# Kernel tuning notes

Hardware: AMD Instinct MI355X
Metric: run time of the kernel (lower is better)

Reference implementation:

```python
import jax, jax.numpy as jnp
import numpy as np

N = 100000
NEG_SLOPE = 0.2
EPS = 1e-16


def _leaky_relu(x):
    return jnp.where(x > 0, x, NEG_SLOPE * x)


def gat_conv(x, src, dst, W, a_src, a_dst, b, heads, out_ch):
    # x: [N, F_in], W: [F_in, heads*out_ch], a_src/a_dst: [heads, out_ch], b: [heads*out_ch]
    h = (x @ W).reshape(N, heads, out_ch)                     # [N, H, C]
    alpha_s = jnp.einsum('nhc,hc->nh', h, a_src)              # [N, H]
    alpha_d = jnp.einsum('nhc,hc->nh', h, a_dst)              # [N, H]
    e = _leaky_relu(alpha_s[src] + alpha_d[dst])              # [E, H]
    # softmax over incoming edges per destination node
    m = jax.ops.segment_max(e, dst, num_segments=N)           # [N, H]
    ee = jnp.exp(e - m[dst])
    denom = jax.ops.segment_sum(ee, dst, num_segments=N)      # [N, H]
    alpha = ee / (denom[dst] + EPS)                           # [E, H]
    msg = h[src] * alpha[:, :, None]                          # [E, H, C]
    out = jax.ops.segment_sum(msg, dst, num_segments=N)       # [N, H, C]
    return out.reshape(N, heads * out_ch) + b


def setup_inputs() -> dict:
    key = jax.random.key(0)
    ks = jax.random.split(key, 16)
    x = jax.random.normal(ks[0], (N, 128), dtype=jnp.float32)
    edge_index = jax.random.randint(ks[1], (2, 1600000), 0, N, dtype=jnp.int64)
    s = 0.1
    return {
        'x': x,
        'edge_index': edge_index,
        'W0': jax.random.normal(ks[2], (128, 4 * 32), dtype=jnp.float32) * s,
        'asrc0': jax.random.normal(ks[3], (4, 32), dtype=jnp.float32) * s,
        'adst0': jax.random.normal(ks[4], (4, 32), dtype=jnp.float32) * s,
        'b0': jnp.zeros((128,), dtype=jnp.float32),
        'W1': jax.random.normal(ks[5], (128, 4 * 32), dtype=jnp.float32) * s,
        'asrc1': jax.random.normal(ks[6], (4, 32), dtype=jnp.float32) * s,
        'adst1': jax.random.normal(ks[7], (4, 32), dtype=jnp.float32) * s,
        'b1': jnp.zeros((128,), dtype=jnp.float32),
        'W2': jax.random.normal(ks[8], (128, 1 * 32), dtype=jnp.float32) * s,
        'asrc2': jax.random.normal(ks[9], (1, 32), dtype=jnp.float32) * s,
        'adst2': jax.random.normal(ks[10], (1, 32), dtype=jnp.float32) * s,
        'b2': jnp.zeros((32,), dtype=jnp.float32),
    }


def reference(x, edge_index, W0, asrc0, adst0, b0, W1, asrc1, adst1, b1, W2, asrc2, adst2, b2):
    # PyG GATConv default add_self_loops=True
    loops = jnp.arange(N, dtype=edge_index.dtype)
    src = jnp.concatenate([edge_index[0], loops])
    dst = jnp.concatenate([edge_index[1], loops])
    # dropout layers are identity in eval mode
    h = gat_conv(x, src, dst, W0, asrc0, adst0, b0, heads=4, out_ch=32)
    h = jax.nn.relu(h)
    h = gat_conv(h, src, dst, W1, asrc1, adst1, b1, heads=4, out_ch=32)
    h = jax.nn.relu(h)
    out = gat_conv(h, src, dst, W2, asrc2, adst2, b2, heads=1, out_ch=32)
    return out
```

## Files before the change

### kernel.cpp

```cpp
#include <hip/hip_runtime.h>
#include <hip/hip_fp16.h>

#define NEG_SLOPE 0.2f
#define EPSV 1e-16f
#define NXCD 8
#define BCAP2 448
#define EPB 8192

typedef _Float16 half8 __attribute__((ext_vector_type(8)));
typedef _Float16 half4v __attribute__((ext_vector_type(4)));
typedef float floatx4 __attribute__((ext_vector_type(4)));

__device__ __forceinline__ float leaky_relu(float v) {
    return v > 0.f ? v : NEG_SLOPE * v;
}

__global__ __launch_bounds__(256)
void wconv3_kernel(const float* __restrict__ W0, const float* __restrict__ W1,
                   const float* __restrict__ W2, __half* __restrict__ Wt0,
                   __half* __restrict__ Wt1, __half* __restrict__ Wt2)
{
    const int idx = blockIdx.x * 256 + threadIdx.x;
    if (idx < 16384) {
        const int k = idx >> 7, c = idx & 127;
        Wt0[c * 128 + k] = __float2half(W0[idx]);
    } else if (idx < 32768) {
        const int i = idx - 16384;
        const int k = i >> 7, c = i & 127;
        Wt1[c * 128 + k] = __float2half(W1[i]);
    } else if (idx < 36864) {
        const int i = idx - 32768;
        const int k = i >> 5, c = i & 31;
        Wt2[c * 128 + k] = __float2half(W2[i]);
    }
}

template<int HC, typename XT>
__global__ __launch_bounds__(256)
void mfma_gemm_kernel(const XT* __restrict__ X, const __half* __restrict__ Wt,
                      const float* __restrict__ asrc, const float* __restrict__ adst,
                      __half* __restrict__ Hout, float* __restrict__ as_,
                      float* __restrict__ ad_, int nrows)
{
    constexpr int NH = HC / 32;
    const int wid = (blockIdx.x * 256 + threadIdx.x) >> 6;
    const int lane = threadIdx.x & 63;
    const int row0 = wid * 16;
    if (row0 >= nrows) return;
    const int r = lane & 15;
    const int kq = lane >> 4;
    const int arow = min(row0 + r, nrows - 1);

    half8 a[4];
    #pragma unroll
    for (int kk = 0; kk < 4; ++kk) {
        const int k0 = kk * 32 + kq * 8;
        if constexpr (sizeof(XT) == 4) {
            const float4 f0 = *(const float4*)&X[(size_t)arow * 128 + k0];
            const float4 f1 = *(const float4*)&X[(size_t)arow * 128 + k0 + 4];
            half8 v;
            v[0] = (_Float16)f0.x; v[1] = (_Float16)f0.y;
            v[2] = (_Float16)f0.z; v[3] = (_Float16)f0.w;
            v[4] = (_Float16)f1.x; v[5] = (_Float16)f1.y;
            v[6] = (_Float16)f1.z; v[7] = (_Float16)f1.w;
            a[kk] = v;
        } else {
            a[kk] = *(const half8*)&X[(size_t)arow * 128 + k0];
        }
    }

    float asp[NH][4];
    float adp[NH][4];
    #pragma unroll
    for (int hh = 0; hh < NH; ++hh)
        #pragma unroll
        for (int j = 0; j < 4; ++j) { asp[hh][j] = 0.f; adp[hh][j] = 0.f; }

    #pragma unroll
    for (int ct = 0; ct < HC / 16; ++ct) {
        floatx4 acc = {0.f, 0.f, 0.f, 0.f};
        #pragma unroll
        for (int kk = 0; kk < 4; ++kk) {
            const half8 b = *(const half8*)&Wt[(size_t)(ct * 16 + r) * 128 + kk * 32 + kq * 8];
            acc = __builtin_amdgcn_mfma_f32_16x16x32_f16(a[kk], b, acc, 0, 0, 0);
        }
        const float avs = asrc[ct * 16 + r];
        const float avd = adst[ct * 16 + r];
        #pragma unroll
        for (int j = 0; j < 4; ++j) {
            asp[ct / 2][j] = fmaf(acc[j], avs, asp[ct / 2][j]);
            adp[ct / 2][j] = fmaf(acc[j], avd, adp[ct / 2][j]);
        }
        #pragma unroll
        for (int j = 0; j < 4; ++j) {
            const int orow = row0 + kq * 4 + j;
            if (orow < nrows)
                Hout[(size_t)orow * HC + ct * 16 + r] = __float2half(acc[j]);
        }
    }

    #pragma unroll
    for (int off = 1; off < 16; off <<= 1) {
        #pragma unroll
        for (int hh = 0; hh < NH; ++hh)
            #pragma unroll
            for (int j = 0; j < 4; ++j) {
                asp[hh][j] += __shfl_xor(asp[hh][j], off);
                adp[hh][j] += __shfl_xor(adp[hh][j], off);
            }
    }
    if constexpr (NH == 4) {
        #pragma unroll
        for (int j = 0; j < 4; ++j) {
            const int row = row0 + kq * 4 + j;
            if (row < nrows) {
                #pragma unroll
                for (int hh = 0; hh < 4; ++hh) {
                    if (r == j * 4 + hh) {
                        as_[row * 4 + hh] = asp[hh][j];
                        ad_[row * 4 + hh] = adp[hh][j];
                    }
                }
            }
        }
    } else {
        #pragma unroll
        for (int j = 0; j < 4; ++j) {
            const int row = row0 + kq * 4 + j;
            if (row < nrows) {
                if (r == j)     as_[row] = asp[0][j];
                if (r == j + 8) ad_[row] = adp[0][j];
            }
        }
    }
}

__global__ __launch_bounds__(256)
void bucket_append_kernel(const int* __restrict__ srcs, const int* __restrict__ dsts,
                          int E, int NB, int* __restrict__ bcur,
                          unsigned* __restrict__ packed)
{
    __shared__ int hist[1024];
    __shared__ int cursor[1024];
    const int t = threadIdx.x;
    const int xcd = blockIdx.x & (NXCD - 1);
    const int base = blockIdx.x * EPB;

    for (int i = t; i < NB; i += 256) hist[i] = 0;
    __syncthreads();
    for (int k = 0; k < EPB / 256; ++k) {
        const int e = base + k * 256 + t;
        if (e < E) atomicAdd(&hist[dsts[e] >> 7], 1);
    }
    __syncthreads();
    for (int i = t; i < NB; i += 256) {
        const int c = hist[i];
        cursor[i] = (c > 0) ? atomicAdd(&bcur[i * NXCD + xcd], c) : 0;
    }
    __syncthreads();
    for (int k = 0; k < EPB / 256; ++k) {
        const int e = base + k * 256 + t;
        if (e < E) {
            const int s = srcs[e];
            const int d = dsts[e];
            const int b = d >> 7;
            const int p = atomicAdd(&cursor[b], 1);
            if (p < BCAP2)
                packed[(size_t)(b * NXCD + xcd) * BCAP2 + p] =
                    (unsigned)s | ((unsigned)(d & 127) << 20);
        }
    }
}

__global__ __launch_bounds__(256)
void bucket_count_kernel(const unsigned* __restrict__ packed, const int* __restrict__ bcur,
                         int* __restrict__ counts, int N)
{
    __shared__ int cnt[128];
    const int t = threadIdx.x;
    const int b = blockIdx.x;
    const int nbase = b * 128;
    if (t < 128) cnt[t] = 1;
    __syncthreads();
    for (int x = 0; x < NXCD; ++x) {
        const int sb = b * NXCD + x;
        const int n = min(bcur[sb], BCAP2);
        const unsigned* bp = packed + (size_t)sb * BCAP2;
        for (int i = t; i < n; i += 256)
            atomicAdd(&cnt[bp[i] >> 20], 1);
    }
    __syncthreads();
    if (t < 128 && nbase + t < N) counts[nbase + t] = cnt[t];
}

__global__ __launch_bounds__(256)
void scan1_kernel(const int* __restrict__ in, int* __restrict__ out,
                  int* __restrict__ bsums, int n)
{
    __shared__ int lds[256];
    const int t = threadIdx.x;
    const int base = blockIdx.x * 1024 + t * 4;
    int v0 = 0, v1 = 0, v2 = 0, v3 = 0;
    if (base + 0 < n) v0 = in[base + 0];
    if (base + 1 < n) v1 = in[base + 1];
    if (base + 2 < n) v2 = in[base + 2];
    if (base + 3 < n) v3 = in[base + 3];
    const int tsum = v0 + v1 + v2 + v3;
    lds[t] = tsum;
    __syncthreads();
    for (int off = 1; off < 256; off <<= 1) {
        const int y = (t >= off) ? lds[t - off] : 0;
        __syncthreads();
        lds[t] += y;
        __syncthreads();
    }
    int excl = lds[t] - tsum;
    if (t == 255) bsums[blockIdx.x] = lds[255];
    if (base + 0 < n) out[base + 0] = excl; excl += v0;
    if (base + 1 < n) out[base + 1] = excl; excl += v1;
    if (base + 2 < n) out[base + 2] = excl; excl += v2;
    if (base + 3 < n) out[base + 3] = excl;
}

__global__ __launch_bounds__(256)
void scan2_kernel(int* __restrict__ bsums, int nb)
{
    __shared__ int lds[256];
    const int t = threadIdx.x;
    const int v = (t < nb) ? bsums[t] : 0;
    lds[t] = v;
    __syncthreads();
    for (int off = 1; off < 256; off <<= 1) {
        const int y = (t >= off) ? lds[t - off] : 0;
        __syncthreads();
        lds[t] += y;
        __syncthreads();
    }
    if (t < nb) bsums[t] = lds[t] - v;
}

__global__ __launch_bounds__(256)
void scan3_kernel(int* __restrict__ row_ptr, const int* __restrict__ bsums,
                  int n, int etot)
{
    const int idx = blockIdx.x * 256 + threadIdx.x;
    if (idx < n) row_ptr[idx] += bsums[idx >> 10];
    if (idx == n) row_ptr[n] = etot;
}

__global__ __launch_bounds__(256)
void bucket_scatter_kernel(const unsigned* __restrict__ packed, const int* __restrict__ bcur,
                           const int* __restrict__ row_ptr, int* __restrict__ col, int N)
{
    __shared__ int cur[128];
    const int t = threadIdx.x;
    const int b = blockIdx.x;
    const int nbase = b * 128;
    if (t < 128 && nbase + t < N) cur[t] = row_ptr[nbase + t];
    __syncthreads();
    if (t < 128 && nbase + t < N) {
        const int p = atomicAdd(&cur[t], 1);
        col[p] = nbase + t;
    }
    for (int x = 0; x < NXCD; ++x) {
        const int sb = b * NXCD + x;
        const int n = min(bcur[sb], BCAP2);
        const unsigned* bp = packed + (size_t)sb * BCAP2;
        for (int i = t; i < n; i += 256) {
            const unsigned en = bp[i];
            const int p = atomicAdd(&cur[en >> 20], 1);
            col[p] = en & 0xFFFFF;
        }
    }
}

template<int H>
__global__ __launch_bounds__(256)
void gather_kernel(const int* __restrict__ row_ptr, const int* __restrict__ col,
                   const float* __restrict__ as_, const float* __restrict__ ad_,
                   const __half* __restrict__ hbuf, const float* __restrict__ bias,
                   __half* __restrict__ hin, float* __restrict__ outf, int N)
{
    __shared__ float pS[4][64 * H];
    __shared__ int   sS[4][64];
    const int w = threadIdx.x >> 6;
    const int lane = threadIdx.x & 63;
    const int d = blockIdx.x * 4 + w;
    if (d >= N) return;
    const int jb = __builtin_amdgcn_readfirstlane(row_ptr[d]);
    const int je = __builtin_amdgcn_readfirstlane(row_ptr[d + 1]);

    float ad0 = 0.f, ad1 = 0.f, ad2 = 0.f, ad3 = 0.f;
    if (H == 4) {
        const float4 adv = *(const float4*)&ad_[d * 4];
        ad0 = adv.x; ad1 = adv.y; ad2 = adv.z; ad3 = adv.w;
    } else {
        ad0 = ad_[d];
    }

    float s0 = 0.f, s1 = 0.f, s2 = 0.f, s3 = 0.f;
    float a0 = 0.f, a1 = 0.f, a2 = 0.f, a3 = 0.f;
    float a4 = 0.f, a5 = 0.f, a6 = 0.f, a7 = 0.f;
    const int q4 = lane >> 4;
    const int cq = lane & 15;
    const int h4 = cq >> 2;
    const int q8 = lane >> 3;
    const int c8 = (lane & 7) * 4;

    for (int cb = jb; cb < je; cb += 64) {
        const int j = cb + lane;
        const int cnt = min(64, je - cb);
        int sreg = 0;
        float p0 = 0.f, p1 = 0.f, p2 = 0.f, p3 = 0.f;
        if (j < je) {
            sreg = col[j];
            if (H == 4) {
                const float4 a = *(const float4*)&as_[sreg * 4];
                p0 = __expf(leaky_relu(a.x + ad0)); s0 += p0;
                p1 = __expf(leaky_relu(a.y + ad1)); s1 += p1;
                p2 = __expf(leaky_relu(a.z + ad2)); s2 += p2;
                p3 = __expf(leaky_relu(a.w + ad3)); s3 += p3;
            } else {
                p0 = __expf(leaky_relu(as_[sreg] + ad0)); s0 += p0;
            }
        }
        __builtin_amdgcn_wave_barrier();
        sS[w][lane] = sreg;
        if (H == 4) {
            *(float4*)&pS[w][lane * 4] = make_float4(p0, p1, p2, p3);
        } else {
            pS[w][lane] = p0;
        }
        __builtin_amdgcn_wave_barrier();
        if (H == 4) {
            #pragma unroll 4
            for (int e2 = q4; e2 < cnt; e2 += 4) {
                const int s2v = sS[w][e2];
                const float pp = pS[w][e2 * 4 + h4];
                const half8 v = *(const half8*)&hbuf[(size_t)s2v * 128 + cq * 8];
                a0 = fmaf(pp, (float)v[0], a0);
                a1 = fmaf(pp, (float)v[1], a1);
                a2 = fmaf(pp, (float)v[2], a2);
                a3 = fmaf(pp, (float)v[3], a3);
                a4 = fmaf(pp, (float)v[4], a4);
                a5 = fmaf(pp, (float)v[5], a5);
                a6 = fmaf(pp, (float)v[6], a6);
                a7 = fmaf(pp, (float)v[7], a7);
            }
        } else {
            #pragma unroll 4
            for (int e2 = q8; e2 < cnt; e2 += 8) {
                const int s2v = sS[w][e2];
                const float pp = pS[w][e2];
                const half4v v = *(const half4v*)&hbuf[(size_t)s2v * 32 + c8];
                a0 = fmaf(pp, (float)v[0], a0);
                a1 = fmaf(pp, (float)v[1], a1);
                a2 = fmaf(pp, (float)v[2], a2);
                a3 = fmaf(pp, (float)v[3], a3);
            }
        }
        __builtin_amdgcn_wave_barrier();
    }

    #pragma unroll
    for (int off = 32; off >= 1; off >>= 1) {
        s0 += __shfl_xor(s0, off);
        if (H == 4) {
            s1 += __shfl_xor(s1, off);
            s2 += __shfl_xor(s2, off);
            s3 += __shfl_xor(s3, off);
        }
    }
    if (H == 4) {
        a0 += __shfl_xor(a0, 16); a0 += __shfl_xor(a0, 32);
        a1 += __shfl_xor(a1, 16); a1 += __shfl_xor(a1, 32);
        a2 += __shfl_xor(a2, 16); a2 += __shfl_xor(a2, 32);
        a3 += __shfl_xor(a3, 16); a3 += __shfl_xor(a3, 32);
        a4 += __shfl_xor(a4, 16); a4 += __shfl_xor(a4, 32);
        a5 += __shfl_xor(a5, 16); a5 += __shfl_xor(a5, 32);
        a6 += __shfl_xor(a6, 16); a6 += __shfl_xor(a6, 32);
        a7 += __shfl_xor(a7, 16); a7 += __shfl_xor(a7, 32);
        if (lane < 16) {
            const float sh = (h4 == 0) ? s0 : (h4 == 1) ? s1 : (h4 == 2) ? s2 : s3;
            const float inv = 1.f / (sh + EPSV);
            const int c0 = cq * 8;
            const float4 b0v = *(const float4*)&bias[c0];
            const float4 b1v = *(const float4*)&bias[c0 + 4];
            union { __half2 h2[4]; float4 f4; } u;
            u.h2[0] = __floats2half2_rn(fmaxf(fmaf(a0, inv, b0v.x), 0.f),
                                        fmaxf(fmaf(a1, inv, b0v.y), 0.f));
            u.h2[1] = __floats2half2_rn(fmaxf(fmaf(a2, inv, b0v.z), 0.f),
                                        fmaxf(fmaf(a3, inv, b0v.w), 0.f));
            u.h2[2] = __floats2half2_rn(fmaxf(fmaf(a4, inv, b1v.x), 0.f),
                                        fmaxf(fmaf(a5, inv, b1v.y), 0.f));
            u.h2[3] = __floats2half2_rn(fmaxf(fmaf(a6, inv, b1v.z), 0.f),
                                        fmaxf(fmaf(a7, inv, b1v.w), 0.f));
            *(float4*)&hin[(size_t)d * 128 + c0] = u.f4;
        }
    } else {
        a0 += __shfl_xor(a0, 8); a0 += __shfl_xor(a0, 16); a0 += __shfl_xor(a0, 32);
        a1 += __shfl_xor(a1, 8); a1 += __shfl_xor(a1, 16); a1 += __shfl_xor(a1, 32);
        a2 += __shfl_xor(a2, 8); a2 += __shfl_xor(a2, 16); a2 += __shfl_xor(a2, 32);
        a3 += __shfl_xor(a3, 8); a3 += __shfl_xor(a3, 16); a3 += __shfl_xor(a3, 32);
        if (lane < 8) {
            const float inv = 1.f / (s0 + EPSV);
            const float4 bb = *(const float4*)&bias[c8];
            *(float4*)&outf[(size_t)d * 32 + c8] =
                make_float4(fmaf(a0, inv, bb.x), fmaf(a1, inv, bb.y),
                            fmaf(a2, inv, bb.z), fmaf(a3, inv, bb.w));
        }
    }
}

extern "C" void kernel_launch(void* const* d_in, const int* in_sizes, int n_in,
                              void* d_out, int out_size, void* d_ws, size_t ws_size,
                              hipStream_t stream)
{
    const float* x     = (const float*)d_in[0];
    const int*   ei    = (const int*)d_in[1];
    const float* W0    = (const float*)d_in[2];
    const float* asrc0 = (const float*)d_in[3];
    const float* adst0 = (const float*)d_in[4];
    const float* b0    = (const float*)d_in[5];
    const float* W1    = (const float*)d_in[6];
    const float* asrc1 = (const float*)d_in[7];
    const float* adst1 = (const float*)d_in[8];
    const float* b1    = (const float*)d_in[9];
    const float* W2    = (const float*)d_in[10];
    const float* asrc2 = (const float*)d_in[11];
    const float* adst2 = (const float*)d_in[12];
    const float* b2    = (const float*)d_in[13];

    const int N = in_sizes[0] / 128;
    const int E = in_sizes[1] / 2;
    const int Etot = E + N;
    const int NB = (N + 127) / 128;
    const int* srcs = ei;
    const int* dsts = ei + E;

    __half* hbuf    = (__half*)d_ws;
    __half* hin     = hbuf + (size_t)N * 128;
    float* as_      = (float*)(hin + (size_t)N * 128);
    float* ad_      = as_ + (size_t)N * 4;
    __half* Wt0     = (__half*)(ad_ + (size_t)N * 4);
    __half* Wt1     = Wt0 + 128 * 128;
    __half* Wt2     = Wt1 + 128 * 128;
    int* counts     = (int*)(Wt2 + 32 * 128);
    int* row_ptr    = counts + N;
    int* bsums      = row_ptr + N + 1;
    int* col        = bsums + 256;
    int* bcur       = col + Etot;
    unsigned* packed = (unsigned*)(bcur + NB * NXCD);

    const dim3 blk(256);
    const int gemm_grid    = ((N + 15) / 16 + 3) / 4;
    const int append_grid  = (E + EPB - 1) / EPB;
    const int gather_grid  = (N + 3) / 4;
    const int nb1          = (N + 1023) / 1024;

    wconv3_kernel<<<(36864 + 255) / 256, blk, 0, stream>>>(W0, W1, W2, Wt0, Wt1, Wt2);
    hipMemsetAsync(bcur, 0, (size_t)NB * NXCD * 4, stream);
    bucket_append_kernel<<<append_grid, blk, 0, stream>>>(srcs, dsts, E, NB, bcur, packed);
    bucket_count_kernel<<<NB, blk, 0, stream>>>(packed, bcur, counts, N);
    scan1_kernel<<<nb1, blk, 0, stream>>>(counts, row_ptr, bsums, N);
    scan2_kernel<<<1, blk, 0, stream>>>(bsums, nb1);
    scan3_kernel<<<(N + 1 + 255) / 256, blk, 0, stream>>>(row_ptr, bsums, N, Etot);
    bucket_scatter_kernel<<<NB, blk, 0, stream>>>(packed, bcur, row_ptr, col, N);

    mfma_gemm_kernel<128, float><<<gemm_grid, blk, 0, stream>>>(
        x, Wt0, asrc0, adst0, hbuf, as_, ad_, N);
    gather_kernel<4><<<gather_grid, blk, 0, stream>>>(row_ptr, col, as_, ad_, hbuf, b0, hin, nullptr, N);

    mfma_gemm_kernel<128, __half><<<gemm_grid, blk, 0, stream>>>(
        hin, Wt1, asrc1, adst1, hbuf, as_, ad_, N);
    gather_kernel<4><<<gather_grid, blk, 0, stream>>>(row_ptr, col, as_, ad_, hbuf, b1, hin, nullptr, N);

    mfma_gemm_kernel<32, __half><<<gemm_grid, blk, 0, stream>>>(
        hin, Wt2, asrc2, adst2, hbuf, as_, ad_, N);
    gather_kernel<1><<<gather_grid, blk, 0, stream>>>(row_ptr, col, as_, ad_, hbuf, b2, nullptr, (float*)d_out, N);
}
```

Baseline: 370.3 us.

## Fold CSR build into fewer kernels and widen final-layer gather loads

```diff
diff --git a/kernel.cpp b/kernel.cpp
--- a/kernel.cpp
+++ b/kernel.cpp
@@ -8,7 +8,6 @@
 #define EPB 8192
 
 typedef _Float16 half8 __attribute__((ext_vector_type(8)));
-typedef _Float16 half4v __attribute__((ext_vector_type(4)));
 typedef float floatx4 __attribute__((ext_vector_type(4)));
 
 __device__ __forceinline__ float leaky_relu(float v) {
@@ -18,9 +17,11 @@
 __global__ __launch_bounds__(256)
 void wconv3_kernel(const float* __restrict__ W0, const float* __restrict__ W1,
                    const float* __restrict__ W2, __half* __restrict__ Wt0,
-                   __half* __restrict__ Wt1, __half* __restrict__ Wt2)
+                   __half* __restrict__ Wt1, __half* __restrict__ Wt2,
+                   int* __restrict__ bcur, int nbx)
 {
     const int idx = blockIdx.x * 256 + threadIdx.x;
+    if (idx < nbx) bcur[idx] = 0;
     if (idx < 16384) {
         const int k = idx >> 7, c = idx & 127;
         Wt0[c * 128 + k] = __float2half(W0[idx]);
@@ -173,15 +174,55 @@
 }
 
 __global__ __launch_bounds__(256)
-void bucket_count_kernel(const unsigned* __restrict__ packed, const int* __restrict__ bcur,
-                         int* __restrict__ counts, int N)
+void scanB_kernel(const int* __restrict__ bcur, int* __restrict__ bbase,
+                  int* __restrict__ row_ptr, int NB, int N)
+{
+    __shared__ int lds[256];
+    const int t = threadIdx.x;
+    int v0 = 0, v1 = 0, v2 = 0, v3 = 0;
+    #pragma unroll
+    for (int j = 0; j < 4; ++j) {
+        const int i = t * 4 + j;
+        int s = 0;
+        if (i < NB) {
+            s = min(128, N - i * 128);
+            #pragma unroll
+            for (int x = 0; x < NXCD; ++x)
+                s += min(bcur[i * NXCD + x], BCAP2);
+        }
+        if (j == 0) v0 = s; else if (j == 1) v1 = s; else if (j == 2) v2 = s; else v3 = s;
+    }
+    const int tsum = v0 + v1 + v2 + v3;
+    lds[t] = tsum;
+    __syncthreads();
+    for (int off = 1; off < 256; off <<= 1) {
+        const int y = (t >= off) ? lds[t - off] : 0;
+        __syncthreads();
+        lds[t] += y;
+        __syncthreads();
+    }
+    int excl = lds[t] - tsum;
+    if (t * 4 + 0 < NB) bbase[t * 4 + 0] = excl; excl += v0;
+    if (t * 4 + 1 < NB) bbase[t * 4 + 1] = excl; excl += v1;
+    if (t * 4 + 2 < NB) bbase[t * 4 + 2] = excl; excl += v2;
+    if (t * 4 + 3 < NB) bbase[t * 4 + 3] = excl;
+    if (t == 255) row_ptr[N] = lds[255];
+}
+
+__global__ __launch_bounds__(256)
+void bucket_scatter_kernel(const unsigned* __restrict__ packed, const int* __restrict__ bcur,
+                           const int* __restrict__ bbase, int* __restrict__ row_ptr,
+                           int* __restrict__ col, int N)
 {
     __shared__ int cnt[128];
+    __shared__ int cur[128];
     const int t = threadIdx.x;
     const int b = blockIdx.x;
     const int nbase = b * 128;
-    if (t < 128) cnt[t] = 1;
-    __syncthreads();
+    const int nvalid = min(128, N - nbase);
+    if (t < 128) cnt[t] = (t < nvalid) ? 1 : 0;
+    __syncthreads();
+    #pragma unroll
     for (int x = 0; x < NXCD; ++x) {
         const int sb = b * NXCD + x;
         const int n = min(bcur[sb], BCAP2);
@@ -190,78 +231,27 @@
             atomicAdd(&cnt[bp[i] >> 20], 1);
     }
     __syncthreads();
-    if (t < 128 && nbase + t < N) counts[nbase + t] = cnt[t];
-}
-
-__global__ __launch_bounds__(256)
-void scan1_kernel(const int* __restrict__ in, int* __restrict__ out,
-                  int* __restrict__ bsums, int n)
-{
-    __shared__ int lds[256];
-    const int t = threadIdx.x;
-    const int base = blockIdx.x * 1024 + t * 4;
-    int v0 = 0, v1 = 0, v2 = 0, v3 = 0;
-    if (base + 0 < n) v0 = in[base + 0];
-    if (base + 1 < n) v1 = in[base + 1];
-    if (base + 2 < n) v2 = in[base + 2];
-    if (base + 3 < n) v3 = in[base + 3];
-    const int tsum = v0 + v1 + v2 + v3;
-    lds[t] = tsum;
-    __syncthreads();
-    for (int off = 1; off < 256; off <<= 1) {
-        const int y = (t >= off) ? lds[t - off] : 0;
+    int myc = 0;
+    if (t < 128) { myc = cnt[t]; cur[t] = myc; }
+    __syncthreads();
+    for (int off = 1; off < 128; off <<= 1) {
+        int y = 0;
+        if (t < 128 && t >= off) y = cur[t - off];
         __syncthreads();
-        lds[t] += y;
+        if (t < 128) cur[t] += y;
         __syncthreads();
     }
-    int excl = lds[t] - tsum;
-    if (t == 255) bsums[blockIdx.x] = lds[255];
-    if (base + 0 < n) out[base + 0] = excl; excl += v0;
-    if (base + 1 < n) out[base + 1] = excl; excl += v1;
-    if (base + 2 < n) out[base + 2] = excl; excl += v2;
-    if (base + 3 < n) out[base + 3] = excl;
-}
-
-__global__ __launch_bounds__(256)
-void scan2_kernel(int* __restrict__ bsums, int nb)
-{
-    __shared__ int lds[256];
-    const int t = threadIdx.x;
-    const int v = (t < nb) ? bsums[t] : 0;
-    lds[t] = v;
-    __syncthreads();
-    for (int off = 1; off < 256; off <<= 1) {
-        const int y = (t >= off) ? lds[t - off] : 0;
-        __syncthreads();
-        lds[t] += y;
-        __syncthreads();
-    }
-    if (t < nb) bsums[t] = lds[t] - v;
-}
-
-__global__ __launch_bounds__(256)
-void scan3_kernel(int* __restrict__ row_ptr, const int* __restrict__ bsums,
-                  int n, int etot)
-{
-    const int idx = blockIdx.x * 256 + threadIdx.x;
-    if (idx < n) row_ptr[idx] += bsums[idx >> 10];
-    if (idx == n) row_ptr[n] = etot;
-}
-
-__global__ __launch_bounds__(256)
-void bucket_scatter_kernel(const unsigned* __restrict__ packed, const int* __restrict__ bcur,
-                           const int* __restrict__ row_ptr, int* __restrict__ col, int N)
-{
-    __shared__ int cur[128];
-    const int t = threadIdx.x;
-    const int b = blockIdx.x;
-    const int nbase = b * 128;
-    if (t < 128 && nbase + t < N) cur[t] = row_ptr[nbase + t];
-    __syncthreads();
-    if (t < 128 && nbase + t < N) {
+    if (t < 128) {
+        const int base = bbase[b] + cur[t] - myc;
+        if (t < nvalid) row_ptr[nbase + t] = base;
+        cur[t] = base;
+    }
+    __syncthreads();
+    if (t < nvalid) {
         const int p = atomicAdd(&cur[t], 1);
         col[p] = nbase + t;
     }
+    #pragma unroll
     for (int x = 0; x < NXCD; ++x) {
         const int sb = b * NXCD + x;
         const int n = min(bcur[sb], BCAP2);
@@ -304,8 +294,8 @@
     const int q4 = lane >> 4;
     const int cq = lane & 15;
     const int h4 = cq >> 2;
-    const int q8 = lane >> 3;
-    const int c8 = (lane & 7) * 4;
+    const int q16 = lane >> 2;
+    const int c16 = (lane & 3) * 8;
 
     for (int cb = jb; cb < je; cb += 64) {
         const int j = cb + lane;
@@ -349,14 +339,18 @@
             }
         } else {
             #pragma unroll 4
-            for (int e2 = q8; e2 < cnt; e2 += 8) {
+            for (int e2 = q16; e2 < cnt; e2 += 16) {
                 const int s2v = sS[w][e2];
                 const float pp = pS[w][e2];
-                const half4v v = *(const half4v*)&hbuf[(size_t)s2v * 32 + c8];
+                const half8 v = *(const half8*)&hbuf[(size_t)s2v * 32 + c16];
                 a0 = fmaf(pp, (float)v[0], a0);
                 a1 = fmaf(pp, (float)v[1], a1);
                 a2 = fmaf(pp, (float)v[2], a2);
                 a3 = fmaf(pp, (float)v[3], a3);
+                a4 = fmaf(pp, (float)v[4], a4);
+                a5 = fmaf(pp, (float)v[5], a5);
+                a6 = fmaf(pp, (float)v[6], a6);
+                a7 = fmaf(pp, (float)v[7], a7);
             }
         }
         __builtin_amdgcn_wave_barrier();
@@ -398,16 +392,24 @@
             *(float4*)&hin[(size_t)d * 128 + c0] = u.f4;
         }
     } else {
-        a0 += __shfl_xor(a0, 8); a0 += __shfl_xor(a0, 16); a0 += __shfl_xor(a0, 32);
-        a1 += __shfl_xor(a1, 8); a1 += __shfl_xor(a1, 16); a1 += __shfl_xor(a1, 32);
-        a2 += __shfl_xor(a2, 8); a2 += __shfl_xor(a2, 16); a2 += __shfl_xor(a2, 32);
-        a3 += __shfl_xor(a3, 8); a3 += __shfl_xor(a3, 16); a3 += __shfl_xor(a3, 32);
-        if (lane < 8) {
+        a0 += __shfl_xor(a0, 4); a0 += __shfl_xor(a0, 8); a0 += __shfl_xor(a0, 16); a0 += __shfl_xor(a0, 32);
+        a1 += __shfl_xor(a1, 4); a1 += __shfl_xor(a1, 8); a1 += __shfl_xor(a1, 16); a1 += __shfl_xor(a1, 32);
+        a2 += __shfl_xor(a2, 4); a2 += __shfl_xor(a2, 8); a2 += __shfl_xor(a2, 16); a2 += __shfl_xor(a2, 32);
+        a3 += __shfl_xor(a3, 4); a3 += __shfl_xor(a3, 8); a3 += __shfl_xor(a3, 16); a3 += __shfl_xor(a3, 32);
+        a4 += __shfl_xor(a4, 4); a4 += __shfl_xor(a4, 8); a4 += __shfl_xor(a4, 16); a4 += __shfl_xor(a4, 32);
+        a5 += __shfl_xor(a5, 4); a5 += __shfl_xor(a5, 8); a5 += __shfl_xor(a5, 16); a5 += __shfl_xor(a5, 32);
+        a6 += __shfl_xor(a6, 4); a6 += __shfl_xor(a6, 8); a6 += __shfl_xor(a6, 16); a6 += __shfl_xor(a6, 32);
+        a7 += __shfl_xor(a7, 4); a7 += __shfl_xor(a7, 8); a7 += __shfl_xor(a7, 16); a7 += __shfl_xor(a7, 32);
+        if (lane < 4) {
             const float inv = 1.f / (s0 + EPSV);
-            const float4 bb = *(const float4*)&bias[c8];
-            *(float4*)&outf[(size_t)d * 32 + c8] =
-                make_float4(fmaf(a0, inv, bb.x), fmaf(a1, inv, bb.y),
-                            fmaf(a2, inv, bb.z), fmaf(a3, inv, bb.w));
+            const float4 bb0 = *(const float4*)&bias[c16];
+            const float4 bb1 = *(const float4*)&bias[c16 + 4];
+            *(float4*)&outf[(size_t)d * 32 + c16] =
+                make_float4(fmaf(a0, inv, bb0.x), fmaf(a1, inv, bb0.y),
+                            fmaf(a2, inv, bb0.z), fmaf(a3, inv, bb0.w));
+            *(float4*)&outf[(size_t)d * 32 + c16 + 4] =
+                make_float4(fmaf(a4, inv, bb1.x), fmaf(a5, inv, bb1.y),
+                            fmaf(a6, inv, bb1.z), fmaf(a7, inv, bb1.w));
         }
     }
 }
@@ -445,10 +447,9 @@
     __half* Wt0     = (__half*)(ad_ + (size_t)N * 4);
     __half* Wt1     = Wt0 + 128 * 128;
     __half* Wt2     = Wt1 + 128 * 128;
-    int* counts     = (int*)(Wt2 + 32 * 128);
-    int* row_ptr    = counts + N;
-    int* bsums      = row_ptr + N + 1;
-    int* col        = bsums + 256;
+    int* row_ptr    = (int*)(Wt2 + 32 * 128);
+    int* bbase      = row_ptr + N + 1;
+    int* col        = bbase + NB;
     int* bcur       = col + Etot;
     unsigned* packed = (unsigned*)(bcur + NB * NXCD);
 
@@ -456,16 +457,12 @@
     const int gemm_grid    = ((N + 15) / 16 + 3) / 4;
     const int append_grid  = (E + EPB - 1) / EPB;
     const int gather_grid  = (N + 3) / 4;
-    const int nb1          = (N + 1023) / 1024;
-
-    wconv3_kernel<<<(36864 + 255) / 256, blk, 0, stream>>>(W0, W1, W2, Wt0, Wt1, Wt2);
-    hipMemsetAsync(bcur, 0, (size_t)NB * NXCD * 4, stream);
+
+    wconv3_kernel<<<(36864 + 255) / 256, blk, 0, stream>>>(W0, W1, W2, Wt0, Wt1, Wt2,
+                                                           bcur, NB * NXCD);
     bucket_append_kernel<<<append_grid, blk, 0, stream>>>(srcs, dsts, E, NB, bcur, packed);
-    bucket_count_kernel<<<NB, blk, 0, stream>>>(packed, bcur, counts, N);
-    scan1_kernel<<<nb1, blk, 0, stream>>>(counts, row_ptr, bsums, N);
-    scan2_kernel<<<1, blk, 0, stream>>>(bsums, nb1);
-    scan3_kernel<<<(N + 1 + 255) / 256, blk, 0, stream>>>(row_ptr, bsums, N, Etot);
-    bucket_scatter_kernel<<<NB, blk, 0, stream>>>(packed, bcur, row_ptr, col, N);
+    scanB_kernel<<<1, blk, 0, stream>>>(bcur, bbase, row_ptr, NB, N);
+    bucket_scatter_kernel<<<NB, blk, 0, stream>>>(packed, bcur, bbase, row_ptr, col, N);
 
     mfma_gemm_kernel<128, float><<<gemm_grid, blk, 0, stream>>>(
         x, Wt0, asrc0, adst0, hbuf, as_, ad_, N);
```

After: 363.5 us. No clear change (-1.8%).
